# Kernel optimization log

Measured on AMD Instinct MI355X. Metric: run time of the kernel, lower is better.

Reference implementation:

```python
import jax, jax.numpy as jnp
import numpy as np

N = 100000      # nodes per node type
E = 1600000     # edges per edge type
IN = 256        # input feature dim
OC = 64         # out_channels
H = 8           # heads
C = OC // H     # hid_dim per head
SLOPE = 0.2


def setup_inputs() -> dict:
    key = jax.random.key(0)
    ks = jax.random.split(key, 24)
    inp = {
        "x_author": jax.random.normal(ks[0], (N, IN), dtype=jnp.float32),
        "x_paper": jax.random.normal(ks[1], (N, IN), dtype=jnp.float32),
        "ei_ap": jax.random.randint(ks[2], (2, E), 0, N, dtype=jnp.int32),
        "ei_pa": jax.random.randint(ks[3], (2, E), 0, N, dtype=jnp.int32),
        "ei_aa": jax.random.randint(ks[4], (2, E), 0, N, dtype=jnp.int32),
        "ei_pp": jax.random.randint(ks[5], (2, E), 0, N, dtype=jnp.int32),
        # per-node-type projections: in_dim -> hid_dim (= C)
        "W_fc_author": jax.random.normal(ks[6], (IN, C), dtype=jnp.float32) * 0.06,
        "b_fc_author": jnp.zeros((C,), dtype=jnp.float32),
        "W_fc_paper": jax.random.normal(ks[7], (IN, C), dtype=jnp.float32) * 0.06,
        "b_fc_paper": jnp.zeros((C,), dtype=jnp.float32),
        # per-edge-type GAT params, stacked over the 4 edge types
        "gat_Wsrc": jax.random.normal(ks[8], (4, C, H * C), dtype=jnp.float32) * 0.35,
        "gat_Wdst": jax.random.normal(ks[9], (4, C, H * C), dtype=jnp.float32) * 0.35,
        "gat_att_src": jax.random.normal(ks[10], (4, H, C), dtype=jnp.float32) * 0.35,
        "gat_att_dst": jax.random.normal(ks[11], (4, H, C), dtype=jnp.float32) * 0.35,
        "gat_bias": jnp.zeros((4, H * C), dtype=jnp.float32),
        # semantic attention params
        "W_k": jax.random.normal(ks[12], (OC, OC), dtype=jnp.float32) * 0.125,
        "b_k": jnp.zeros((OC,), dtype=jnp.float32),
        "q": jax.random.normal(ks[13], (OC,), dtype=jnp.float32),
    }
    return inp


def _gat(h_src, h_dst, ei, Ws, Wd, a_s, a_d, b):
    # h_src: [Ns, C], h_dst: [Nd, C], ei: [2, E] (row 0 = src idx, row 1 = dst idx)
    n_dst = h_dst.shape[0]
    xs = (h_src @ Ws).reshape(-1, H, C)               # [Ns, H, C]
    xd = (h_dst @ Wd).reshape(-1, H, C)               # [Nd, H, C]
    alpha_s = (xs * a_s).sum(-1)                      # [Ns, H]
    alpha_d = (xd * a_d).sum(-1)                      # [Nd, H]
    src, dst = ei[0], ei[1]
    e = jax.nn.leaky_relu(alpha_s[src] + alpha_d[dst], SLOPE)   # [E, H]
    # segment softmax over incoming edges of each target node
    m = jax.ops.segment_max(e, dst, num_segments=n_dst)         # [Nd, H]
    w = jnp.exp(e - m[dst])                                      # [E, H]
    z = jax.ops.segment_sum(w, dst, num_segments=n_dst)         # [Nd, H]
    alpha = w / (z[dst] + 1e-16)                                 # [E, H]
    msg = xs[src] * alpha[:, :, None]                            # [E, H, C]
    out = jax.ops.segment_sum(msg, dst, num_segments=n_dst)     # [Nd, H, C]
    return out.reshape(n_dst, H * C) + b                         # [Nd, OC]


def _semantic(outs, W_k, b_k, q):
    xs = jnp.stack(outs, axis=0)                       # [M, N, OC]
    key = jnp.tanh(xs @ W_k + b_k).mean(axis=1)        # [M, OC]
    score = jax.nn.softmax((q * key).sum(-1), axis=0)  # [M]
    return (xs * score[:, None, None]).sum(0)          # [N, OC]


def reference(x_author, x_paper, ei_ap, ei_pa, ei_aa, ei_pp,
              W_fc_author, b_fc_author, W_fc_paper, b_fc_paper,
              gat_Wsrc, gat_Wdst, gat_att_src, gat_att_dst, gat_bias,
              W_k, b_k, q):
    h_a = x_author @ W_fc_author + b_fc_author   # [N, C]
    h_p = x_paper @ W_fc_paper + b_fc_paper      # [N, C]
    # edge types: 0 a->p, 1 p->a, 2 a->a, 3 p->p
    out_p_ap = _gat(h_a, h_p, ei_ap, gat_Wsrc[0], gat_Wdst[0], gat_att_src[0], gat_att_dst[0], gat_bias[0])
    out_a_pa = _gat(h_p, h_a, ei_pa, gat_Wsrc[1], gat_Wdst[1], gat_att_src[1], gat_att_dst[1], gat_bias[1])
    out_a_aa = _gat(h_a, h_a, ei_aa, gat_Wsrc[2], gat_Wdst[2], gat_att_src[2], gat_att_dst[2], gat_bias[2])
    out_p_pp = _gat(h_p, h_p, ei_pp, gat_Wsrc[3], gat_Wdst[3], gat_att_src[3], gat_att_dst[3], gat_bias[3])
    out_a = _semantic([out_a_pa, out_a_aa], W_k, b_k, q)   # insertion order: pa, aa
    out_p = _semantic([out_p_ap, out_p_pp], W_k, b_k, q)   # insertion order: ap, pp
    return jnp.stack([out_a, out_p], axis=0)               # [2, N, OC]
```

## Files before the change

### kernel.cpp

```cpp
#include <hip/hip_runtime.h>
#include <hip/hip_fp16.h>
#include <math.h>

#define NN 100000
#define EE 1600000
#define IND 256
#define SLOPE 0.2f

#define BUKBITS 9
#define BUKSZ 512
#define NBUK 196
#define CAP 8960
#define CHUNK 4096
#define BINBLK 391
#define NODEBLK 391
#define SKB3 256
#define SKTILES 6250

typedef float f4 __attribute__((ext_vector_type(4)));
typedef _Float16 h2 __attribute__((ext_vector_type(2)));
typedef _Float16 h8 __attribute__((ext_vector_type(8)));
typedef float fx4 __attribute__((ext_vector_type(4)));

__global__ __launch_bounds__(512) void prep_V(
    const float* __restrict__ Ws, const float* __restrict__ as_,
    const float* __restrict__ Wd, const float* __restrict__ ad_,
    float* __restrict__ Vs, float* __restrict__ Vd) {
  int t = threadIdx.x;
  int half = t >> 8;
  int r = t & 255;
  int et = r >> 6, k = (r >> 3) & 7, hh = r & 7;
  const float* W = half ? Wd : Ws;
  const float* a = half ? ad_ : as_;
  float acc = 0.f;
#pragma unroll
  for (int c = 0; c < 8; ++c)
    acc += W[et * 512 + k * 64 + hh * 8 + c] * a[et * 64 + hh * 8 + c];
  (half ? Vd : Vs)[et * 64 + k * 8 + hh] = acc;
}

__device__ __forceinline__ void unpack8(const f4& raw, float* hs) {
  union { f4 v; __half2 p[4]; } u;
  u.v = raw;
#pragma unroll
  for (int j = 0; j < 4; ++j) {
    float2 f = __half22float2(u.p[j]);
    hs[2 * j] = f.x;
    hs[2 * j + 1] = f.y;
  }
}

__global__ __launch_bounds__(256) void fc_kernel(
    const float* __restrict__ xa, const float* __restrict__ xp,
    const float* __restrict__ Wa, const float* __restrict__ ba,
    const float* __restrict__ Wp, const float* __restrict__ bp,
    f4* __restrict__ h16) {
  __shared__ float sW[IND * 8];
  __shared__ float sB[8];
  int bid = blockIdx.x;
  int type = bid >= NODEBLK;
  int lrow = (type ? bid - NODEBLK : bid) * 256 + threadIdx.x;
  const float* W = type ? Wp : Wa;
  const float* bb = type ? bp : ba;
  for (int i = threadIdx.x; i < IND * 8; i += 256) sW[i] = W[i];
  if (threadIdx.x < 8) sB[threadIdx.x] = bb[threadIdx.x];
  __syncthreads();
  if (lrow >= NN) return;
  const float* x = (type ? xp : xa) + (size_t)lrow * IND;
  float acc[8];
#pragma unroll
  for (int c = 0; c < 8; ++c) acc[c] = sB[c];
#pragma unroll 4
  for (int k4 = 0; k4 < IND / 4; ++k4) {
    float4 xv = ((const float4*)x)[k4];
    float xk[4] = {xv.x, xv.y, xv.z, xv.w};
#pragma unroll
    for (int kk = 0; kk < 4; ++kk) {
      const float* wr = &sW[(k4 * 4 + kk) * 8];
#pragma unroll
      for (int c = 0; c < 8; ++c) acc[c] = fmaf(xk[kk], wr[c], acc[c]);
    }
  }
  union { f4 v; __half2 p[4]; } u;
#pragma unroll
  for (int c = 0; c < 4; ++c)
    u.p[c] = __floats2half2_rn(acc[2 * c], acc[2 * c + 1]);
  h16[(size_t)type * NN + lrow] = u.v;
}

__global__ __launch_bounds__(256) void bin_kernel(
    const int* __restrict__ e0, const int* __restrict__ e1,
    const int* __restrict__ e2, const int* __restrict__ e3,
    int* __restrict__ gcur, int* __restrict__ edge_src) {
  __shared__ int s_pack[CHUNK];
  __shared__ unsigned char s_buk[CHUNK];
  __shared__ int s_hist[NBUK], s_base[NBUK], s_cur[NBUK];
  int et = blockIdx.y;
  const int* ei = et == 0 ? e0 : et == 1 ? e1 : et == 2 ? e2 : e3;
  int t = threadIdx.x;
  for (int b = t; b < NBUK; b += 256) { s_hist[b] = 0; s_cur[b] = 0; }
  __syncthreads();
  int base = blockIdx.x * CHUNK;
#pragma unroll
  for (int r = 0; r < CHUNK / 256; ++r) {
    int i = r * 256 + t;
    int e = base + i;
    int bk = 255;
    if (e < EE) {
      int s = __builtin_nontemporal_load(ei + e);
      int d = __builtin_nontemporal_load(ei + EE + e);
      s_pack[i] = s | ((d & (BUKSZ - 1)) << 17);
      bk = d >> BUKBITS;
      atomicAdd(&s_hist[bk], 1);
    }
    s_buk[i] = (unsigned char)bk;
  }
  __syncthreads();
  for (int b = t; b < NBUK; b += 256)
    s_base[b] = atomicAdd(&gcur[et * NBUK + b], s_hist[b]);
  __syncthreads();
#pragma unroll
  for (int r = 0; r < CHUNK / 256; ++r) {
    int i = r * 256 + t;
    int bk = s_buk[i];
    if (bk != 255) {
      int pos = s_base[bk] + atomicAdd(&s_cur[bk], 1);
      if (pos < CAP)
        edge_src[(size_t)(et * NBUK + bk) * CAP + pos] = s_pack[i];
    }
  }
}

__global__ __launch_bounds__(256) void csr_kernel(
    const int* __restrict__ gcur, int* __restrict__ edge_src,
    int* __restrict__ counts, int* __restrict__ rowptr) {
  __shared__ int s_data[CAP];
  __shared__ int s_hist[BUKSZ], s_off[BUKSZ], s_part[256];
  int buk = blockIdx.x, et = blockIdx.y, t = threadIdx.x;
  int bsz = gcur[et * NBUK + buk];
  if (bsz > CAP) bsz = CAP;
  int ebase = (et * NBUK + buk) * CAP;
  for (int j = t; j < BUKSZ; j += 256) s_hist[j] = 0;
  __syncthreads();
  for (int i = t; i < bsz; i += 256) {
    int v = __builtin_nontemporal_load(edge_src + ebase + i);
    s_data[i] = v;
    atomicAdd(&s_hist[v >> 17], 1);
  }
  __syncthreads();
  int b2 = t * 2;
  int a0 = s_hist[b2], a1 = s_hist[b2 + 1];
  int tot = a0 + a1;
  s_part[t] = tot;
  __syncthreads();
#pragma unroll
  for (int off = 1; off < 256; off <<= 1) {
    int v = (t >= off) ? s_part[t - off] : 0;
    __syncthreads();
    s_part[t] += v;
    __syncthreads();
  }
  int ex = s_part[t] - tot;
  s_off[b2] = ex;
  s_off[b2 + 1] = ex + a0;
  __syncthreads();
  for (int j = t; j < BUKSZ; j += 256) {
    int node = buk * BUKSZ + j;
    if (node < NN) {
      counts[(size_t)et * NN + node] = s_hist[j];
      rowptr[(size_t)et * NN + node] = ebase + s_off[j];
    }
  }
  __syncthreads();
  for (int i = t; i < bsz; i += 256) {
    int v = s_data[i];
    int pos = atomicAdd(&s_off[v >> 17], 1);
    edge_src[ebase + pos] = v & 0x1FFFF;
  }
}

__device__ __forceinline__ void gat_edge16(
    const f4& raw, const float* __restrict__ Vse,
    const float ad[8], float g[64], float z[8]) {
  float hs[8];
  unpack8(raw, hs);
#pragma unroll
  for (int hh = 0; hh < 8; ++hh) {
    float e = ad[hh];
#pragma unroll
    for (int k = 0; k < 8; ++k) e = fmaf(hs[k], Vse[k * 8 + hh], e);
    e = e > 0.f ? e : SLOPE * e;
    float w = __expf(e);
    z[hh] += w;
#pragma unroll
    for (int k = 0; k < 8; ++k) g[hh * 8 + k] = fmaf(w, hs[k], g[hh * 8 + k]);
  }
}

__global__ __launch_bounds__(256) void gat_pull(
    const f4* __restrict__ h16,
    const int* __restrict__ rowptr, const int* __restrict__ counts,
    const int* __restrict__ edge_src,
    const float* __restrict__ Wsrc_all, const float* __restrict__ Vs,
    const float* __restrict__ Vd,
    const float* __restrict__ bias_all, f4* __restrict__ out16) {
  int b = blockIdx.x;
  int xcd = b & 7;
  int g_ = xcd >> 2;
  int sid = (b >> 3) * 4 + (xcd & 3);
  if (sid >= 2 * NODEBLK) return;
  int et = (sid < NODEBLK) ? g_ : g_ + 2;
  int nb = (sid < NODEBLK) ? sid : sid - NODEBLK;
  int n = nb * 256 + threadIdx.x;
  if (n >= NN) return;
  int st = et & 1;
  int dt = (et & 1) ^ (et < 2 ? 1 : 0);
  const f4* hsrc = h16 + (size_t)st * NN;
  const f4* hdst = h16 + (size_t)dt * NN;
  const float* Ws = Wsrc_all + et * 512;
  const float* Vse = Vs + et * 64;
  const float* Vde = Vd + et * 64;
  const float* bs = bias_all + et * 64;

  float hd[8];
  unpack8(hdst[n], hd);
  float ad[8];
#pragma unroll
  for (int hh = 0; hh < 8; ++hh) {
    float acc = 0.f;
#pragma unroll
    for (int k = 0; k < 8; ++k) acc = fmaf(hd[k], Vde[k * 8 + hh], acc);
    ad[hh] = acc;
  }
  float g[64];
  float z[8];
#pragma unroll
  for (int i = 0; i < 64; ++i) g[i] = 0.f;
#pragma unroll
  for (int hh = 0; hh < 8; ++hh) z[hh] = 0.f;

  int start = rowptr[(size_t)et * NN + n];
  int deg = counts[(size_t)et * NN + n];
  const int* es = edge_src + start;
  int i = 0;
#pragma unroll 1
  for (; i + 4 <= deg; i += 4) {
    int s0 = __builtin_nontemporal_load(es + i);
    int s1 = __builtin_nontemporal_load(es + i + 1);
    int s2 = __builtin_nontemporal_load(es + i + 2);
    int s3 = __builtin_nontemporal_load(es + i + 3);
    f4 r0 = hsrc[s0];
    f4 r1 = hsrc[s1];
    f4 r2 = hsrc[s2];
    f4 r3 = hsrc[s3];
    gat_edge16(r0, Vse, ad, g, z);
    gat_edge16(r1, Vse, ad, g, z);
    gat_edge16(r2, Vse, ad, g, z);
    gat_edge16(r3, Vse, ad, g, z);
  }
#pragma unroll 1
  for (; i < deg; ++i) {
    int s = __builtin_nontemporal_load(es + i);
    f4 r = hsrc[s];
    gat_edge16(r, Vse, ad, g, z);
  }

  f4* op = out16 + ((size_t)et * NN + n) * 8;
#pragma unroll
  for (int hh = 0; hh < 8; ++hh) {
    float rz = 1.f / (z[hh] + 1e-16f);
    float o[8];
#pragma unroll
    for (int c = 0; c < 8; ++c) {
      float acc = 0.f;
#pragma unroll
      for (int k = 0; k < 8; ++k)
        acc = fmaf(g[hh * 8 + k], Ws[k * 64 + hh * 8 + c], acc);
      o[c] = acc * rz + bs[hh * 8 + c];
    }
    union { f4 v; __half2 p[4]; } u;
#pragma unroll
    for (int c = 0; c < 4; ++c)
      u.p[c] = __floats2half2_rn(o[2 * c], o[2 * c + 1]);
    op[hh] = u.v;
  }
}

__global__ __launch_bounds__(256) void semantic_key(
    const f4* __restrict__ out16, const float* __restrict__ Wk,
    const float* __restrict__ bk, float* __restrict__ key) {
  __shared__ float s_red[4][64];
  int m = blockIdx.y;
  int t = threadIdx.x;
  int lane = t & 63;
  int w = t >> 6;
  int kg = lane >> 4;
  int col = lane & 15;
  h8 bfrag[2][4];
#pragma unroll
  for (int ks = 0; ks < 2; ++ks)
#pragma unroll
    for (int jt = 0; jt < 4; ++jt) {
      h8 bf;
#pragma unroll
      for (int i = 0; i < 8; ++i)
        bf[i] = (_Float16)Wk[(ks * 32 + kg * 8 + i) * 64 + jt * 16 + col];
      bfrag[ks][jt] = bf;
    }
  float bkv[4];
#pragma unroll
  for (int jt = 0; jt < 4; ++jt) bkv[jt] = bk[jt * 16 + col];
  float kacc[4] = {0.f, 0.f, 0.f, 0.f};
  const f4* base = out16 + (size_t)m * NN * 8;
  int gw = blockIdx.x * 4 + w;
#pragma unroll 1
  for (int tile = gw; tile < SKTILES; tile += SKB3 * 4) {
    union { f4 v; h8 h; } a0u, a1u;
    const f4* rowp = base + (size_t)(tile * 16 + col) * 8;
    a0u.v = rowp[kg];
    a1u.v = rowp[4 + kg];
#pragma unroll
    for (int jt = 0; jt < 4; ++jt) {
      fx4 d = {0.f, 0.f, 0.f, 0.f};
      d = __builtin_amdgcn_mfma_f32_16x16x32_f16(a0u.h, bfrag[0][jt], d, 0, 0, 0);
      d = __builtin_amdgcn_mfma_f32_16x16x32_f16(a1u.h, bfrag[1][jt], d, 0, 0, 0);
#pragma unroll
      for (int r = 0; r < 4; ++r) {
        float x = d[r] + bkv[jt];
        kacc[jt] += 1.f - 2.f / (__expf(2.f * x) + 1.f);
      }
    }
  }
#pragma unroll
  for (int jt = 0; jt < 4; ++jt) {
    kacc[jt] += __shfl_xor(kacc[jt], 16, 64);
    kacc[jt] += __shfl_xor(kacc[jt], 32, 64);
  }
  if (lane < 16) {
#pragma unroll
    for (int jt = 0; jt < 4; ++jt) s_red[w][jt * 16 + col] = kacc[jt];
  }
  __syncthreads();
  if (t < 64) {
    float v = s_red[0][t] + s_red[1][t] + s_red[2][t] + s_red[3][t];
    atomicAdd(&key[m * 64 + t], v);
  }
}

__global__ __launch_bounds__(64) void scores_k(
    const float* __restrict__ key, const float* __restrict__ q,
    float* __restrict__ wsc) {
  int l = threadIdx.x;
  float qv = q[l];
  float d[4];
#pragma unroll
  for (int m = 0; m < 4; ++m) {
    float p = qv * key[m * 64 + l];
#pragma unroll
    for (int off = 32; off; off >>= 1) p += __shfl_xor(p, off, 64);
    d[m] = p * (1.0f / NN);
  }
  if (l == 0) {
    {
      float mx = fmaxf(d[1], d[2]);
      float e1 = __expf(d[1] - mx), e2 = __expf(d[2] - mx);
      float inv = 1.f / (e1 + e2);
      wsc[1] = e1 * inv;
      wsc[2] = e2 * inv;
    }
    {
      float mx = fmaxf(d[0], d[3]);
      float e0 = __expf(d[0] - mx), e3 = __expf(d[3] - mx);
      float inv = 1.f / (e0 + e3);
      wsc[0] = e0 * inv;
      wsc[3] = e3 * inv;
    }
  }
}

__global__ __launch_bounds__(256) void combine_kernel(
    const f4* __restrict__ out16, const float* __restrict__ wsc,
    float* __restrict__ out) {
  size_t i8 = (size_t)blockIdx.x * 256 + threadIdx.x;
  if (i8 >= (size_t)2 * NN * 8) return;
  int type = i8 >= (size_t)NN * 8;
  size_t r8 = type ? i8 - (size_t)NN * 8 : i8;
  int m0 = type ? 0 : 1;
  int m1 = type ? 3 : 2;
  float s0 = wsc[m0], s1 = wsc[m1];
  f4 a = __builtin_nontemporal_load(out16 + (size_t)m0 * NN * 8 + r8);
  f4 b = __builtin_nontemporal_load(out16 + (size_t)m1 * NN * 8 + r8);
  float av[8], bv[8];
  unpack8(a, av);
  unpack8(b, bv);
  float4 o0, o1;
  o0.x = s0 * av[0] + s1 * bv[0];
  o0.y = s0 * av[1] + s1 * bv[1];
  o0.z = s0 * av[2] + s1 * bv[2];
  o0.w = s0 * av[3] + s1 * bv[3];
  o1.x = s0 * av[4] + s1 * bv[4];
  o1.y = s0 * av[5] + s1 * bv[5];
  o1.z = s0 * av[6] + s1 * bv[6];
  o1.w = s0 * av[7] + s1 * bv[7];
  ((float4*)out)[i8 * 2] = o0;
  ((float4*)out)[i8 * 2 + 1] = o1;
}

extern "C" void kernel_launch(void* const* d_in, const int* in_sizes, int n_in,
                              void* d_out, int out_size, void* d_ws,
                              size_t ws_size, hipStream_t stream) {
  const float* x_a = (const float*)d_in[0];
  const float* x_p = (const float*)d_in[1];
  const int* ei0 = (const int*)d_in[2];
  const int* ei1 = (const int*)d_in[3];
  const int* ei2 = (const int*)d_in[4];
  const int* ei3 = (const int*)d_in[5];
  const float* Wfa = (const float*)d_in[6];
  const float* bfa = (const float*)d_in[7];
  const float* Wfp = (const float*)d_in[8];
  const float* bfp = (const float*)d_in[9];
  const float* gWs = (const float*)d_in[10];
  const float* gWd = (const float*)d_in[11];
  const float* gas = (const float*)d_in[12];
  const float* gad = (const float*)d_in[13];
  const float* gb = (const float*)d_in[14];
  const float* Wk = (const float*)d_in[15];
  const float* bk = (const float*)d_in[16];
  const float* q = (const float*)d_in[17];
  float* out = (float*)d_out;
  (void)in_sizes; (void)n_in; (void)out_size; (void)ws_size;

  float* ws = (float*)d_ws;
  f4* h16 = (f4*)ws;
  f4* out16 = (f4*)(ws + (size_t)2 * NN * 4);
  float* Vs = ws + (size_t)2 * NN * 4 + (size_t)4 * NN * 32;
  float* Vd = Vs + 256;
  float* key = Vd + 256;
  float* wsc = key + 256;
  int* counts = (int*)(wsc + 8);
  int* rowptr = counts + (size_t)4 * NN;
  int* gcur = rowptr + (size_t)4 * NN;
  int* edge_src = gcur + 1024;

  hipMemsetAsync(gcur, 0, 1024 * sizeof(int), stream);
  hipMemsetAsync(key, 0, 256 * sizeof(float), stream);

  prep_V<<<1, 512, 0, stream>>>(gWs, gas, gWd, gad, Vs, Vd);
  fc_kernel<<<2 * NODEBLK, 256, 0, stream>>>(x_a, x_p, Wfa, bfa, Wfp, bfp, h16);
  bin_kernel<<<dim3(BINBLK, 4), 256, 0, stream>>>(ei0, ei1, ei2, ei3, gcur, edge_src);
  csr_kernel<<<dim3(NBUK, 4), 256, 0, stream>>>(gcur, edge_src, counts, rowptr);
  gat_pull<<<1568, 256, 0, stream>>>(h16, rowptr, counts, edge_src,
                                     gWs, Vs, Vd, gb, out16);
  semantic_key<<<dim3(SKB3, 4), 256, 0, stream>>>(out16, Wk, bk, key);
  scores_k<<<1, 64, 0, stream>>>(key, q, wsc);
  combine_kernel<<<(2 * NN * 8 + 255) / 256, 256, 0, stream>>>(out16, wsc, out);
}
```

Before: 297.2 us.

## Compute node-type projection with fp16 MFMA tiles instead of scalar FMAs

Rewrites fc_kernel so each wavefront computes 16-row tiles of x@W using the 16x16x32 fp16 MFMA instruction, with the weights pre-packed into registers and the inputs converted to fp16 on load. Output is staged through shared memory and written as packed half rows. This removes the per-thread 256x8 scalar FMA loop with its strided per-thread row reads, letting lanes read contiguous 8-float chunks. The trade-offs are fp16 rounding of inputs and weights before the matmul, and wasted MFMA columns because only 8 of the 16 are used.

Result: slower. 327.5 us (+10.2%).

```diff
diff --git a/kernel.cpp b/kernel.cpp
--- a/kernel.cpp
+++ b/kernel.cpp
@@ -16,6 +16,8 @@
 #define NODEBLK 391
 #define SKB3 256
 #define SKTILES 6250
+#define FCTILES 12500
+#define FCBLK 1563
 
 typedef float f4 __attribute__((ext_vector_type(4)));
 typedef _Float16 h2 __attribute__((ext_vector_type(2)));
@@ -55,37 +57,59 @@
     const float* __restrict__ Wa, const float* __restrict__ ba,
     const float* __restrict__ Wp, const float* __restrict__ bp,
     f4* __restrict__ h16) {
-  __shared__ float sW[IND * 8];
-  __shared__ float sB[8];
-  int bid = blockIdx.x;
-  int type = bid >= NODEBLK;
-  int lrow = (type ? bid - NODEBLK : bid) * 256 + threadIdx.x;
-  const float* W = type ? Wp : Wa;
-  const float* bb = type ? bp : ba;
-  for (int i = threadIdx.x; i < IND * 8; i += 256) sW[i] = W[i];
-  if (threadIdx.x < 8) sB[threadIdx.x] = bb[threadIdx.x];
-  __syncthreads();
-  if (lrow >= NN) return;
-  const float* x = (type ? xp : xa) + (size_t)lrow * IND;
-  float acc[8];
-#pragma unroll
-  for (int c = 0; c < 8; ++c) acc[c] = sB[c];
-#pragma unroll 4
-  for (int k4 = 0; k4 < IND / 4; ++k4) {
-    float4 xv = ((const float4*)x)[k4];
-    float xk[4] = {xv.x, xv.y, xv.z, xv.w};
-#pragma unroll
-    for (int kk = 0; kk < 4; ++kk) {
-      const float* wr = &sW[(k4 * 4 + kk) * 8];
-#pragma unroll
-      for (int c = 0; c < 8; ++c) acc[c] = fmaf(xk[kk], wr[c], acc[c]);
-    }
-  }
-  union { f4 v; __half2 p[4]; } u;
-#pragma unroll
-  for (int c = 0; c < 4; ++c)
-    u.p[c] = __floats2half2_rn(acc[2 * c], acc[2 * c + 1]);
-  h16[(size_t)type * NN + lrow] = u.v;
+  __shared__ _Float16 sT[4][16][8];
+  int t = threadIdx.x;
+  int lane = t & 63;
+  int w = t >> 6;
+  int kg = lane >> 4;
+  int col = lane & 15;
+  h8 bfA[8], bfP[8];
+#pragma unroll
+  for (int ks = 0; ks < 8; ++ks) {
+    h8 a, p;
+#pragma unroll
+    for (int i = 0; i < 8; ++i) {
+      int k = ks * 32 + kg * 8 + i;
+      a[i] = (col < 8) ? (_Float16)Wa[k * 8 + col] : (_Float16)0.f;
+      p[i] = (col < 8) ? (_Float16)Wp[k * 8 + col] : (_Float16)0.f;
+    }
+    bfA[ks] = a;
+    bfP[ks] = p;
+  }
+  float biasA = (col < 8) ? ba[col] : 0.f;
+  float biasP = (col < 8) ? bp[col] : 0.f;
+  int gw = blockIdx.x * 4 + w;
+#pragma unroll 1
+  for (int ti = 0; ti < 2; ++ti) {
+    int tile = gw * 2 + ti;
+    if (tile >= FCTILES) break;
+    int type = tile >= SKTILES;
+    const float* xrow = (type ? xp : xa) +
+                        (size_t)(tile * 16 - type * NN + col) * IND;
+    fx4 d = {0.f, 0.f, 0.f, 0.f};
+#pragma unroll
+    for (int ks = 0; ks < 8; ++ks) {
+      f4 x0 = *(const f4*)(xrow + ks * 32 + kg * 8);
+      f4 x1 = *(const f4*)(xrow + ks * 32 + kg * 8 + 4);
+      union { h8 h; __half2 p[4]; } au;
+      au.p[0] = __floats2half2_rn(x0.x, x0.y);
+      au.p[1] = __floats2half2_rn(x0.z, x0.w);
+      au.p[2] = __floats2half2_rn(x1.x, x1.y);
+      au.p[3] = __floats2half2_rn(x1.z, x1.w);
+      h8 b = type ? bfP[ks] : bfA[ks];
+      d = __builtin_amdgcn_mfma_f32_16x16x32_f16(au.h, b, d, 0, 0, 0);
+    }
+    float bias = type ? biasP : biasA;
+    if (col < 8) {
+#pragma unroll
+      for (int r = 0; r < 4; ++r)
+        sT[w][kg * 4 + r][col] = (_Float16)(d[r] + bias);
+    }
+    if (lane < 16) {
+      f4 v = *(const f4*)(&sT[w][lane][0]);
+      h16[(size_t)tile * 16 + lane] = v;
+    }
+  }
 }
 
 __global__ __launch_bounds__(256) void bin_kernel(
@@ -446,7 +470,7 @@
   hipMemsetAsync(key, 0, 256 * sizeof(float), stream);
 
   prep_V<<<1, 512, 0, stream>>>(gWs, gas, gWd, gad, Vs, Vd);
-  fc_kernel<<<2 * NODEBLK, 256, 0, stream>>>(x_a, x_p, Wfa, bfa, Wfp, bfp, h16);
+  fc_kernel<<<FCBLK, 256, 0, stream>>>(x_a, x_p, Wfa, bfa, Wfp, bfp, h16);
   bin_kernel<<<dim3(BINBLK, 4), 256, 0, stream>>>(ei0, ei1, ei2, ei3, gcur, edge_src);
   csr_kernel<<<dim3(NBUK, 4), 256, 0, stream>>>(gcur, edge_src, counts, rowptr);
   gat_pull<<<1568, 256, 0, stream>>>(h16, rowptr, counts, edge_src,
```
